# Kernel optimization log

Hardware: AMD Instinct MI355X
Metric: run time of the kernel (lower is better)

Reference implementation:

```python
import jax, jax.numpy as jnp
import numpy as np

DIM = 1024
HEADS = 16
SCALE = DIM ** (-0.5)  # standard_scale=False -> dim**-0.5


def setup_inputs() -> dict:
    key = jax.random.key(0)
    ks = jax.random.split(key, 7)
    B, N, D = 2, 2048, DIM
    x = jax.random.normal(ks[0], (B, N, D), dtype=jnp.float32)
    gamma = jax.random.uniform(ks[1], (B, HEADS), dtype=jnp.float32)
    dist_matrix = jax.random.uniform(ks[2], (N, N), dtype=jnp.float32)
    qkv_w = jax.random.normal(ks[3], (D, 3 * D), dtype=jnp.float32) * (1.0 / np.sqrt(D))
    qkv_b = jnp.zeros((3 * D,), dtype=jnp.float32)
    proj_w = jax.random.normal(ks[4], (D, D), dtype=jnp.float32) * (1.0 / np.sqrt(D))
    proj_b = jnp.zeros((D,), dtype=jnp.float32)
    return {"x": x, "gamma": gamma, "dist_matrix": dist_matrix,
            "qkv_w": qkv_w, "qkv_b": qkv_b, "proj_w": proj_w, "proj_b": proj_b}


def reference(x, gamma, dist_matrix, qkv_w, qkv_b, proj_w, proj_b):
    B, N, D = x.shape
    H = HEADS
    Dh = D // H
    # qkv projection: [B,N,3D] -> [3,B,H,N,Dh]
    qkv = (x @ qkv_w + qkv_b).reshape(B, N, 3, H, Dh).transpose(2, 0, 3, 1, 4)
    q, k, v = qkv[0], qkv[1], qkv[2]
    # scores: [B,H,N,N]
    scores = jnp.einsum("bhnd,bhmd->bhnm", q, k) * SCALE
    # zoom bias: subtract gamma_per_head * distance
    scores = scores - gamma[:, :, None, None] * dist_matrix[None, None]
    attn = jax.nn.softmax(scores, axis=-1)  # dropout=0 (eval)
    out = jnp.einsum("bhnm,bhmd->bhnd", attn, v)
    out = out.transpose(0, 2, 1, 3).reshape(B, N, D)
    return out @ proj_w + proj_b
```

## Files before the change

kernel.cpp:

```cpp
#include <hip/hip_runtime.h>
#include <hip/hip_bf16.h>


typedef __attribute__((ext_vector_type(8))) short bf16x8;
typedef __attribute__((ext_vector_type(4))) float f32x4;
typedef __attribute__((ext_vector_type(16))) float f32x16;
typedef __attribute__((ext_vector_type(4))) unsigned short us4;
typedef __attribute__((ext_vector_type(2))) unsigned int u32x2;

#define MFMA(a, b, c) __builtin_amdgcn_mfma_f32_16x16x32_bf16((a), (b), (c), 0, 0, 0)
#define MFMA32(a, b, c) __builtin_amdgcn_mfma_f32_32x32x16_bf16((a), (b), (c), 0, 0, 0)

__device__ __forceinline__ unsigned short f2bf(float f) {
  unsigned u = __float_as_uint(f);
  u += 0x7fffu + ((u >> 16) & 1u);
  return (unsigned short)(u >> 16);
}

__device__ __forceinline__ unsigned cvtpk_bf16(float lo, float hi) {
  unsigned r;
  asm("v_cvt_pk_bf16_f32 %0, %1, %2" : "=v"(r) : "v"(lo), "v"(hi));
  return r;
}

#define PLSWAP(a, b) asm volatile("v_permlane32_swap_b32 %0, %1" : "+v"(a), "+v"(b))

__device__ __forceinline__ float tree16(const float* p) {
  float t0 = (p[0] + p[1]) + (p[2] + p[3]);
  float t1 = (p[4] + p[5]) + (p[6] + p[7]);
  float t2 = (p[8] + p[9]) + (p[10] + p[11]);
  float t3 = (p[12] + p[13]) + (p[14] + p[15]);
  return (t0 + t1) + (t2 + t3);
}

__global__ __launch_bounds__(256) void k_prep(const float* __restrict__ x,
                                              short* __restrict__ xb,
                                              const float* __restrict__ dist,
                                              unsigned char* __restrict__ dTq8,
                                              const float* __restrict__ qkv_w,
                                              short* __restrict__ wT,
                                              const float* __restrict__ proj_w,
                                              short* __restrict__ pT) {
  __shared__ float t[32][33];
  const int b = blockIdx.x, tid = threadIdx.x;
  if (b < 2048) {
    int i = b * 256 + tid;
    float4 a = ((const float4*)x)[2 * i];
    float4 c = ((const float4*)x)[2 * i + 1];
    us4 lo, hi;
    lo.x = f2bf(a.x); lo.y = f2bf(a.y); lo.z = f2bf(a.z); lo.w = f2bf(a.w);
    hi.x = f2bf(c.x); hi.y = f2bf(c.y); hi.z = f2bf(c.z); hi.w = f2bf(c.w);
    us4* o = (us4*)(xb + 8 * (size_t)i);
    o[0] = lo; o[1] = hi;
    return;
  }
  const int tx = tid & 31, ty = tid >> 5;
  if (b < 6144) {
    int bb = b - 2048;
    int c0 = (bb & 63) * 32, r0 = (bb >> 6) * 32;
#pragma unroll
    for (int j = 0; j < 32; j += 8)
      t[ty + j][tx] = dist[(size_t)(r0 + ty + j) * 2048 + c0 + tx];
    __syncthreads();
#pragma unroll
    for (int j = 0; j < 32; j += 8) {
      int c = c0 + ty + j, q = r0 + tx;
      int u = (int)(t[tx][ty + j] * 256.0f + 0.5f);
      u = u > 255 ? 255 : u;
      dTq8[(size_t)(c >> 2) * 8192 + (size_t)q * 4 + (c & 3)] = (unsigned char)u;
    }
    return;
  }
  if (b < 9216) {
    int bb = b - 6144;
    int c0 = (bb % 96) * 32, r0 = (bb / 96) * 32;
#pragma unroll
    for (int j = 0; j < 32; j += 8)
      t[ty + j][tx] = qkv_w[(size_t)(r0 + ty + j) * 3072 + c0 + tx];
    __syncthreads();
#pragma unroll
    for (int j = 0; j < 32; j += 8)
      wT[(size_t)(c0 + ty + j) * 1024 + r0 + tx] = (short)f2bf(t[tx][ty + j]);
    return;
  }
  {
    int bb = b - 9216;
    int c0 = (bb & 31) * 32, r0 = (bb >> 5) * 32;
#pragma unroll
    for (int j = 0; j < 32; j += 8)
      t[ty + j][tx] = proj_w[(size_t)(r0 + ty + j) * 1024 + c0 + tx];
    __syncthreads();
#pragma unroll
    for (int j = 0; j < 32; j += 8)
      pT[(size_t)(c0 + ty + j) * 1024 + r0 + tx] = (short)f2bf(t[tx][ty + j]);
  }
}

template <int MODE, int BM>
__global__ __launch_bounds__(256) void k_gemm(const short* __restrict__ A,
                                              const short* __restrict__ B,
                                              const float* __restrict__ bias,
                                              void* __restrict__ C0, void* __restrict__ C1,
                                              void* __restrict__ C2, int M, int N, int K) {
  __shared__ __align__(16) short bufA[2][BM * 32];
  __shared__ __align__(16) short bufB[2][128 * 32];
  const int tid = threadIdx.x, lane = tid & 63, wave = tid >> 6;
  const int nwg = gridDim.x * gridDim.y;
  const int wlin = blockIdx.y * gridDim.x + blockIdx.x;
  const int cpx = nwg >> 3;
  const int swzb = (wlin & 7) * cpx + (wlin >> 3);
  const int bx = swzb % gridDim.x, by = swzb / gridDim.x;
  const int m0 = by * BM, n0 = bx * 128;
  const int wm = (BM == 128) ? (wave >> 1) * 64 : 0;
  const int wn = (BM == 128) ? (wave & 1) * 64 : wave * 32;
  const int NI = (BM == 128) ? 4 : 2;
  const int KT = K >> 5;
  f32x4 acc[4][4] = {};

  const short* ga = A + (size_t)m0 * K;
  const short* gb = B + (size_t)n0 * K;

#define STAGE(kt, bsel)                                                                   \
  {                                                                                       \
    const short* pa = ga + (kt) * 32;                                                     \
    const short* pb = gb + (kt) * 32;                                                     \
    _Pragma("unroll") for (int i = 0; i < BM / 64; i++) {                                 \
      int s = i * 256 + tid;                                                              \
      __builtin_amdgcn_global_load_lds(                                                   \
          (const __attribute__((address_space(1))) void*)(pa + (size_t)(s >> 2) * K +     \
                                                          (s & 3) * 8),                   \
          (__attribute__((address_space(3))) void*)(&bufA[bsel][(i * 256 + wave * 64) * 8]), \
          16, 0, 0);                                                                      \
    }                                                                                     \
    _Pragma("unroll") for (int i = 0; i < 2; i++) {                                       \
      int s = i * 256 + tid;                                                              \
      __builtin_amdgcn_global_load_lds(                                                   \
          (const __attribute__((address_space(1))) void*)(pb + (size_t)(s >> 2) * K +     \
                                                          (s & 3) * 8),                   \
          (__attribute__((address_space(3))) void*)(&bufB[bsel][(i * 256 + wave * 64) * 8]), \
          16, 0, 0);                                                                      \
    }                                                                                     \
  }

  STAGE(0, 0)
  for (int kt = 0; kt < KT; ++kt) {
    const int cur = kt & 1;
    __syncthreads();
    if (kt + 1 < KT) STAGE(kt + 1, cur ^ 1)
    bf16x8 af[4], bfr[4];
#pragma unroll
    for (int i = 0; i < 4; i++)
      af[i] = *(const bf16x8*)&bufA[cur][(wm + i * 16 + (lane & 15)) * 32 + (lane >> 4) * 8];
#pragma unroll
    for (int i = 0; i < NI; i++)
      bfr[i] = *(const bf16x8*)&bufB[cur][(wn + i * 16 + (lane & 15)) * 32 + (lane >> 4) * 8];
#pragma unroll
    for (int mi = 0; mi < 4; mi++)
#pragma unroll
      for (int ni = 0; ni < NI; ni++) acc[mi][ni] = MFMA(af[mi], bfr[ni], acc[mi][ni]);
  }
#undef STAGE

#pragma unroll
  for (int mi = 0; mi < 4; mi++)
#pragma unroll
    for (int ni = 0; ni < NI; ni++) {
      int row0 = m0 + wm + mi * 16 + (lane >> 4) * 4;
      int col = n0 + wn + ni * 16 + (lane & 15);
      float bv = bias[col];
      if constexpr (MODE == 0) {
        int which = col >> 10, h = (col >> 6) & 15, d = col & 63;
        int b = row0 >> 11, nt0 = row0 & 2047;
        if (which == 2) {
          us4 pk;
          pk.x = f2bf(acc[mi][ni][0] + bv);
          pk.y = f2bf(acc[mi][ni][1] + bv);
          pk.z = f2bf(acc[mi][ni][2] + bv);
          pk.w = f2bf(acc[mi][ni][3] + bv);
          *(us4*)((short*)C2 + ((size_t)((b << 4) + h) * 64 + d) * 2048 + nt0) = pk;
        } else {
          float sc = (which == 0) ? 0.045084220f : 1.0f;
          short* dst = (which == 0) ? (short*)C0 : (short*)C1;
#pragma unroll
          for (int r = 0; r < 4; r++)
            dst[((size_t)((b << 4) + h) * 2048 + nt0 + r) * 64 + d] =
                (short)f2bf((acc[mi][ni][r] + bv) * sc);
        }
      } else {
        float* o = (float*)C0;
#pragma unroll
        for (int r = 0; r < 4; r++) o[(size_t)(row0 + r) * N + col] = acc[mi][ni][r] + bv;
      }
    }
}

__global__ __launch_bounds__(512, 4) void k_attn(const short* __restrict__ Qb,
                                                 const short* __restrict__ Kb,
                                                 const short* __restrict__ Vt,
                                                 const float* __restrict__ gamma,
                                                 const unsigned char* __restrict__ dTq8,
                                                 short* __restrict__ attn_out) {
  __shared__ __align__(16) short bufK[2][2][64 * 64];
  __shared__ __align__(16) short bufV[2][2][64 * 64];
  __shared__ __align__(16) unsigned char bufD[8][2048];
  const int tid = threadIdx.x;
  const int lane = tid & 63, wave = tid >> 6;
  const int grp = wave >> 2, w4 = wave & 3;
  const int q32 = lane & 31, hl = lane >> 5;
  const int w = blockIdx.x;
  const int xcd = w & 7, idx = w >> 3;
  const int bh = (xcd << 2) | (idx >> 4);
  const int qblock = idx & 15;
  const int qbase = qblock * 128 + w4 * 32;
  const float G2b = gamma[bh] * 1.4426950408889634f * (1.0f / 256.0f);
  const size_t head = (size_t)bh * 2048 * 64;
  const int qrow = qbase + q32;
  const size_t qw4 = (size_t)qblock * 512 + (size_t)w4 * 128;
  const char* kptr = (const char*)(Kb + head);
  const char* vptr = (const char*)(Vt + head);
  const int swz = (q32 & 7) << 4;

  bf16x8 qf[4];
#pragma unroll
  for (int ds = 0; ds < 4; ds++)
    qf[ds] = *(const bf16x8*)&Qb[head + (size_t)qrow * 64 + ds * 16 + hl * 8];

#define STAGEKV(kb, bsel)                                                                  \
  {                                                                                        \
    _Pragma("unroll") for (int i = 0; i < 2; i++) {                                        \
      int s = i * 256 + (tid & 255);                                                       \
      int row = s >> 3, sw = ((s & 7) * 16) ^ ((row & 7) << 4);                            \
      __builtin_amdgcn_global_load_lds(                                                    \
          (const __attribute__((address_space(1))) void*)(kptr + (size_t)(kb) * 128 +      \
                                                          row * 128 + sw),                 \
          (__attribute__((address_space(3))) void*)(&bufK[grp][bsel][(i * 256 + w4 * 64) * 8]),\
          16, 0, 0);                                                                       \
      __builtin_amdgcn_global_load_lds(                                                    \
          (const __attribute__((address_space(1))) void*)(vptr + (size_t)row * 4096 +      \
                                                          (size_t)(kb) * 2 + sw),          \
          (__attribute__((address_space(3))) void*)(&bufV[grp][bsel][(i * 256 + w4 * 64) * 8]),\
          16, 0, 0);                                                                       \
    }                                                                                      \
  }

#define DISTDMA(kb)                                                                        \
  {                                                                                        \
    _Pragma("unroll") for (int j = 0; j < 2; j++) {                                        \
      int s = j * 64 + lane;                                                               \
      int row = s >> 3, cb = (s & 7) * 16;                                                 \
      __builtin_amdgcn_global_load_lds(                                                    \
          (const __attribute__((address_space(1))) void*)(dTq8 +                           \
              (size_t)(((kb) >> 2) + row) * 8192 + qw4 + cb),                              \
          (__attribute__((address_space(3))) void*)(&bufD[wave][j * 1024]), 16, 0, 0);     \
    }                                                                                      \
  }

  float ls = 0.f;
  f32x16 acc0 = {}, acc1 = {};

  STAGEKV(grp * 64, 0)
  DISTDMA(grp * 64)

  const unsigned* ldsD = (const unsigned*)&bufD[wave][0];

  for (int it = 0; it < 16; ++it) {
    const int cur = it & 1;
    const int kb = (2 * it + grp) * 64;
    __syncthreads();

    unsigned dw0[4], dw1[4];
#pragma unroll
    for (int a = 0; a < 4; a++) {
      dw0[a] = ldsD[(2 * a + hl) * 32 + q32];
      dw1[a] = ldsD[(8 + 2 * a + hl) * 32 + q32];
    }
    asm volatile("s_waitcnt lgkmcnt(0)" ::: "memory");
    __builtin_amdgcn_sched_barrier(0);

    if (it + 1 < 16) {
      STAGEKV(kb + 128, cur ^ 1)
      DISTDMA(kb + 128)
    }

    const char* kbase = (const char*)&bufK[grp][cur][0];
    f32x16 s0 = {}, s1 = {};
#pragma unroll
    for (int ds = 0; ds < 4; ds++) {
      int c = (ds * 32 + hl * 16) ^ swz;
      bf16x8 a0 = *(const bf16x8*)(kbase + q32 * 128 + c);
      bf16x8 a1 = *(const bf16x8*)(kbase + (32 + q32) * 128 + c);
      s0 = MFMA32(a0, qf[ds], s0);
      s1 = MFMA32(a1, qf[ds], s1);
    }

    float p0[16], p1[16];
#pragma unroll
    for (int a = 0; a < 4; a++)
#pragma unroll
      for (int b = 0; b < 4; b++) {
        p0[4 * a + b] = __builtin_amdgcn_exp2f(
            s0[4 * a + b] - G2b * (float)((dw0[a] >> (8 * b)) & 255u));
        p1[4 * a + b] = __builtin_amdgcn_exp2f(
            s1[4 * a + b] - G2b * (float)((dw1[a] >> (8 * b)) & 255u));
      }
    ls += tree16(p0) + tree16(p1);

    unsigned P0[4][2], P1[4][2];
#pragma unroll
    for (int a = 0; a < 4; a++)
#pragma unroll
      for (int wd = 0; wd < 2; wd++) {
        P0[a][wd] = cvtpk_bf16(p0[4 * a + 2 * wd], p0[4 * a + 2 * wd + 1]);
        P1[a][wd] = cvtpk_bf16(p1[4 * a + 2 * wd], p1[4 * a + 2 * wd + 1]);
      }
    PLSWAP(P0[0][0], P0[1][0]); PLSWAP(P0[0][1], P0[1][1]);
    PLSWAP(P0[2][0], P0[3][0]); PLSWAP(P0[2][1], P0[3][1]);
    PLSWAP(P1[0][0], P1[1][0]); PLSWAP(P1[0][1], P1[1][1]);
    PLSWAP(P1[2][0], P1[3][0]); PLSWAP(P1[2][1], P1[3][1]);

    union { unsigned u[4]; bf16x8 v; } pf00, pf01, pf10, pf11;
    pf00.u[0] = P0[0][0]; pf00.u[1] = P0[0][1]; pf00.u[2] = P0[1][0]; pf00.u[3] = P0[1][1];
    pf01.u[0] = P0[2][0]; pf01.u[1] = P0[2][1]; pf01.u[2] = P0[3][0]; pf01.u[3] = P0[3][1];
    pf10.u[0] = P1[0][0]; pf10.u[1] = P1[0][1]; pf10.u[2] = P1[1][0]; pf10.u[3] = P1[1][1];
    pf11.u[0] = P1[2][0]; pf11.u[1] = P1[2][1]; pf11.u[2] = P1[3][0]; pf11.u[3] = P1[3][1];

    const char* vbase = (const char*)&bufV[grp][cur][0];
#pragma unroll
    for (int dt = 0; dt < 2; dt++) {
      f32x16* ac = dt ? &acc1 : &acc0;
      int vr = (dt * 32 + q32) * 128;
      bf16x8 v00 = *(const bf16x8*)(vbase + vr + ((0 * 64 + 0 * 32 + hl * 16) ^ swz));
      bf16x8 v01 = *(const bf16x8*)(vbase + vr + ((0 * 64 + 1 * 32 + hl * 16) ^ swz));
      bf16x8 v10 = *(const bf16x8*)(vbase + vr + ((1 * 64 + 0 * 32 + hl * 16) ^ swz));
      bf16x8 v11 = *(const bf16x8*)(vbase + vr + ((1 * 64 + 1 * 32 + hl * 16) ^ swz));
      *ac = MFMA32(v00, pf00.v, *ac);
      *ac = MFMA32(v01, pf01.v, *ac);
      *ac = MFMA32(v10, pf10.v, *ac);
      *ac = MFMA32(v11, pf11.v, *ac);
    }
  }
#undef STAGEKV
#undef DISTDMA

  __syncthreads();
  float* mrg = (float*)&bufK[0][0][0];
  float* mls = (float*)&bufV[0][0][0];
  if (grp == 1) {
    float lsr = ls + __shfl_xor(ls, 32, 64);
    if (hl == 0) mls[w4 * 32 + q32] = lsr;
#pragma unroll
    for (int dt = 0; dt < 2; dt++) {
      const f32x16* ac = dt ? &acc1 : &acc0;
#pragma unroll
      for (int a = 0; a < 4; a++) {
        int chunk = (dt * 8 + a * 2 + hl) ^ (q32 & 15);
        f32x4 v;
        v.x = (*ac)[4 * a + 0]; v.y = (*ac)[4 * a + 1];
        v.z = (*ac)[4 * a + 2]; v.w = (*ac)[4 * a + 3];
        *(f32x4*)((char*)mrg + (w4 * 32 + q32) * 256 + chunk * 16) = v;
      }
    }
  }
  __syncthreads();
  if (grp == 0) {
    const int b_ = bh >> 4, h_ = bh & 15;
    float lsr = ls + __shfl_xor(ls, 32, 64);
    float linv = 1.0f / (lsr + mls[w4 * 32 + q32]);
    size_t base = ((size_t)b_ * 2048 + qrow) * 1024 + h_ * 64;
#pragma unroll
    for (int dt = 0; dt < 2; dt++) {
      const f32x16* ac = dt ? &acc1 : &acc0;
#pragma unroll
      for (int a = 0; a < 4; a++) {
        int chunk = (dt * 8 + a * 2 + hl) ^ (q32 & 15);
        f32x4 vB = *(const f32x4*)((const char*)mrg + (w4 * 32 + q32) * 256 + chunk * 16);
        u32x2 wv;
        wv.x = cvtpk_bf16(((*ac)[4 * a + 0] + vB.x) * linv, ((*ac)[4 * a + 1] + vB.y) * linv);
        wv.y = cvtpk_bf16(((*ac)[4 * a + 2] + vB.z) * linv, ((*ac)[4 * a + 3] + vB.w) * linv);
        *(u32x2*)&attn_out[base + dt * 32 + a * 8 + hl * 4] = wv;
      }
    }
  }
}

extern "C" void kernel_launch(void* const* d_in, const int* in_sizes, int n_in,
                              void* d_out, int out_size, void* d_ws, size_t ws_size,
                              hipStream_t stream) {
  const float* x = (const float*)d_in[0];
  const float* gamma = (const float*)d_in[1];
  const float* dist = (const float*)d_in[2];
  const float* qkv_w = (const float*)d_in[3];
  const float* qkv_b = (const float*)d_in[4];
  const float* proj_w = (const float*)d_in[5];
  const float* proj_b = (const float*)d_in[6];
  float* out = (float*)d_out;

  const size_t MB = 1024 * 1024;
  char* ws = (char*)d_ws;
  short* xb = (short*)(ws + 0 * MB);
  short* wT = (short*)(ws + 8 * MB);
  short* pT = (short*)(ws + 14 * MB);
  short* Qb = (short*)(ws + 16 * MB);
  short* Kb = (short*)(ws + 24 * MB);
  short* Vt = (short*)(ws + 32 * MB);
  unsigned char* dTq8 = (unsigned char*)(ws + 40 * MB);
  short* attn = (short*)(ws + 0 * MB);

  k_prep<<<dim3(10240), dim3(256), 0, stream>>>(x, xb, dist, dTq8, qkv_w, wT, proj_w, pT);
  k_gemm<0, 128><<<dim3(24, 32), dim3(256), 0, stream>>>(xb, wT, qkv_b, Qb, Kb, Vt,
                                                         4096, 3072, 1024);
  k_attn<<<dim3(512), dim3(512), 0, stream>>>(Qb, Kb, Vt, gamma, dTq8, attn);
  k_gemm<1, 64><<<dim3(8, 64), dim3(256), 0, stream>>>(attn, pT, proj_b, out, nullptr, nullptr,
                                                       4096, 1024, 1024);
}
```

Measured before the change: 119.6 us.

## Drop split-K wave groups in attention kernel; each wave walks all keys

The attention kernel previously used 512 threads in two wave groups, each handling half the key blocks, then merged partial accumulators and row sums through LDS. Now each block has 256 threads (4 waves) that iterate over all 32 key blocks alone, with a single double-buffered K/V stage and no cross-group merge. This removes the merge epilogue, two barriers and half the LDS, which may allow more resident blocks. The cost is fewer waves per block and a serial loop twice as long, so there is less latency hiding per query tile.

```diff
diff --git a/kernel.cpp b/kernel.cpp
--- a/kernel.cpp
+++ b/kernel.cpp
@@ -194,28 +194,27 @@
     }
 }
 
-__global__ __launch_bounds__(512, 4) void k_attn(const short* __restrict__ Qb,
+__global__ __launch_bounds__(256, 4) void k_attn(const short* __restrict__ Qb,
                                                  const short* __restrict__ Kb,
                                                  const short* __restrict__ Vt,
                                                  const float* __restrict__ gamma,
                                                  const unsigned char* __restrict__ dTq8,
                                                  short* __restrict__ attn_out) {
-  __shared__ __align__(16) short bufK[2][2][64 * 64];
-  __shared__ __align__(16) short bufV[2][2][64 * 64];
-  __shared__ __align__(16) unsigned char bufD[8][2048];
+  __shared__ __align__(16) short bufK[2][64 * 64];
+  __shared__ __align__(16) short bufV[2][64 * 64];
+  __shared__ __align__(16) unsigned char bufD[4][2048];
   const int tid = threadIdx.x;
   const int lane = tid & 63, wave = tid >> 6;
-  const int grp = wave >> 2, w4 = wave & 3;
   const int q32 = lane & 31, hl = lane >> 5;
   const int w = blockIdx.x;
   const int xcd = w & 7, idx = w >> 3;
   const int bh = (xcd << 2) | (idx >> 4);
   const int qblock = idx & 15;
-  const int qbase = qblock * 128 + w4 * 32;
+  const int qbase = qblock * 128 + wave * 32;
   const float G2b = gamma[bh] * 1.4426950408889634f * (1.0f / 256.0f);
   const size_t head = (size_t)bh * 2048 * 64;
   const int qrow = qbase + q32;
-  const size_t qw4 = (size_t)qblock * 512 + (size_t)w4 * 128;
+  const size_t qw4 = (size_t)qblock * 512 + (size_t)wave * 128;
   const char* kptr = (const char*)(Kb + head);
   const char* vptr = (const char*)(Vt + head);
   const int swz = (q32 & 7) << 4;
@@ -228,17 +227,17 @@
 #define STAGEKV(kb, bsel)                                                                  \
   {                                                                                        \
     _Pragma("unroll") for (int i = 0; i < 2; i++) {                                        \
-      int s = i * 256 + (tid & 255);                                                       \
+      int s = i * 256 + tid;                                                               \
       int row = s >> 3, sw = ((s & 7) * 16) ^ ((row & 7) << 4);                            \
       __builtin_amdgcn_global_load_lds(                                                    \
           (const __attribute__((address_space(1))) void*)(kptr + (size_t)(kb) * 128 +      \
                                                           row * 128 + sw),                 \
-          (__attribute__((address_space(3))) void*)(&bufK[grp][bsel][(i * 256 + w4 * 64) * 8]),\
+          (__attribute__((address_space(3))) void*)(&bufK[bsel][(i * 256 + wave * 64) * 8]),\
           16, 0, 0);                                                                       \
       __builtin_amdgcn_global_load_lds(                                                    \
           (const __attribute__((address_space(1))) void*)(vptr + (size_t)row * 4096 +      \
                                                           (size_t)(kb) * 2 + sw),          \
-          (__attribute__((address_space(3))) void*)(&bufV[grp][bsel][(i * 256 + w4 * 64) * 8]),\
+          (__attribute__((address_space(3))) void*)(&bufV[bsel][(i * 256 + wave * 64) * 8]),\
           16, 0, 0);                                                                       \
     }                                                                                      \
   }
@@ -258,14 +257,14 @@
   float ls = 0.f;
   f32x16 acc0 = {}, acc1 = {};
 
-  STAGEKV(grp * 64, 0)
-  DISTDMA(grp * 64)
+  STAGEKV(0, 0)
+  DISTDMA(0)
 
   const unsigned* ldsD = (const unsigned*)&bufD[wave][0];
 
-  for (int it = 0; it < 16; ++it) {
+  for (int it = 0; it < 32; ++it) {
     const int cur = it & 1;
-    const int kb = (2 * it + grp) * 64;
+    const int kb = it * 64;
     __syncthreads();
 
     unsigned dw0[4], dw1[4];
@@ -277,12 +276,12 @@
     asm volatile("s_waitcnt lgkmcnt(0)" ::: "memory");
     __builtin_amdgcn_sched_barrier(0);
 
-    if (it + 1 < 16) {
-      STAGEKV(kb + 128, cur ^ 1)
-      DISTDMA(kb + 128)
-    }
-
-    const char* kbase = (const char*)&bufK[grp][cur][0];
+    if (it + 1 < 32) {
+      STAGEKV(kb + 64, cur ^ 1)
+      DISTDMA(kb + 64)
+    }
+
+    const char* kbase = (const char*)&bufK[cur][0];
     f32x16 s0 = {}, s1 = {};
 #pragma unroll
     for (int ds = 0; ds < 4; ds++) {
@@ -324,7 +323,7 @@
     pf10.u[0] = P1[0][0]; pf10.u[1] = P1[0][1]; pf10.u[2] = P1[1][0]; pf10.u[3] = P1[1][1];
     pf11.u[0] = P1[2][0]; pf11.u[1] = P1[2][1]; pf11.u[2] = P1[3][0]; pf11.u[3] = P1[3][1];
 
-    const char* vbase = (const char*)&bufV[grp][cur][0];
+    const char* vbase = (const char*)&bufV[cur][0];
 #pragma unroll
     for (int dt = 0; dt < 2; dt++) {
       f32x16* ac = dt ? &acc1 : &acc0;
@@ -342,43 +341,19 @@
 #undef STAGEKV
 #undef DISTDMA
 
-  __syncthreads();
-  float* mrg = (float*)&bufK[0][0][0];
-  float* mls = (float*)&bufV[0][0][0];
-  if (grp == 1) {
-    float lsr = ls + __shfl_xor(ls, 32, 64);
-    if (hl == 0) mls[w4 * 32 + q32] = lsr;
-#pragma unroll
-    for (int dt = 0; dt < 2; dt++) {
-      const f32x16* ac = dt ? &acc1 : &acc0;
-#pragma unroll
-      for (int a = 0; a < 4; a++) {
-        int chunk = (dt * 8 + a * 2 + hl) ^ (q32 & 15);
-        f32x4 v;
-        v.x = (*ac)[4 * a + 0]; v.y = (*ac)[4 * a + 1];
-        v.z = (*ac)[4 * a + 2]; v.w = (*ac)[4 * a + 3];
-        *(f32x4*)((char*)mrg + (w4 * 32 + q32) * 256 + chunk * 16) = v;
-      }
-    }
-  }
-  __syncthreads();
-  if (grp == 0) {
-    const int b_ = bh >> 4, h_ = bh & 15;
-    float lsr = ls + __shfl_xor(ls, 32, 64);
-    float linv = 1.0f / (lsr + mls[w4 * 32 + q32]);
-    size_t base = ((size_t)b_ * 2048 + qrow) * 1024 + h_ * 64;
-#pragma unroll
-    for (int dt = 0; dt < 2; dt++) {
-      const f32x16* ac = dt ? &acc1 : &acc0;
-#pragma unroll
-      for (int a = 0; a < 4; a++) {
-        int chunk = (dt * 8 + a * 2 + hl) ^ (q32 & 15);
-        f32x4 vB = *(const f32x4*)((const char*)mrg + (w4 * 32 + q32) * 256 + chunk * 16);
-        u32x2 wv;
-        wv.x = cvtpk_bf16(((*ac)[4 * a + 0] + vB.x) * linv, ((*ac)[4 * a + 1] + vB.y) * linv);
-        wv.y = cvtpk_bf16(((*ac)[4 * a + 2] + vB.z) * linv, ((*ac)[4 * a + 3] + vB.w) * linv);
-        *(u32x2*)&attn_out[base + dt * 32 + a * 8 + hl * 4] = wv;
-      }
+  const int b_ = bh >> 4, h_ = bh & 15;
+  float lsr = ls + __shfl_xor(ls, 32, 64);
+  float linv = 1.0f / lsr;
+  size_t base = ((size_t)b_ * 2048 + qrow) * 1024 + h_ * 64;
+#pragma unroll
+  for (int dt = 0; dt < 2; dt++) {
+    const f32x16* ac = dt ? &acc1 : &acc0;
+#pragma unroll
+    for (int a = 0; a < 4; a++) {
+      u32x2 wv;
+      wv.x = cvtpk_bf16((*ac)[4 * a + 0] * linv, (*ac)[4 * a + 1] * linv);
+      wv.y = cvtpk_bf16((*ac)[4 * a + 2] * linv, (*ac)[4 * a + 3] * linv);
+      *(u32x2*)&attn_out[base + dt * 32 + a * 8 + hl * 4] = wv;
     }
   }
 }
@@ -409,7 +384,7 @@
   k_prep<<<dim3(10240), dim3(256), 0, stream>>>(x, xb, dist, dTq8, qkv_w, wT, proj_w, pT);
   k_gemm<0, 128><<<dim3(24, 32), dim3(256), 0, stream>>>(xb, wT, qkv_b, Qb, Kb, Vt,
                                                          4096, 3072, 1024);
-  k_attn<<<dim3(512), dim3(512), 0, stream>>>(Qb, Kb, Vt, gamma, dTq8, attn);
+  k_attn<<<dim3(512), dim3(256), 0, stream>>>(Qb, Kb, Vt, gamma, dTq8, attn);
   k_gemm<1, 64><<<dim3(8, 64), dim3(256), 0, stream>>>(attn, pT, proj_b, out, nullptr, nullptr,
                                                        4096, 1024, 1024);
 }
```

Result: slower. 122.5 us (+2.5%).
